# Performance work log

Hardware: AMD Instinct MI355X
Metric: run time of the kernel (lower is better)

## Reference

```python
import jax, jax.numpy as jnp
import numpy as np

N = 6000          # RPN proposals pre-NMS
C = 64            # ROI feature channels
NUM_CLASSES = 21  # VOC-style classes
THR = 0.7         # NMS IoU threshold (generate_rois default)


def setup_inputs() -> dict:
    key = jax.random.key(0)
    k = jax.random.split(key, 8)
    # valid boxes: x1<x2, y1<y2 inside a 1000x1000 image
    xy = jax.random.uniform(k[0], (N, 2)) * 900.0
    wh = jax.random.uniform(k[1], (N, 2)) * 90.0 + 10.0
    boxes = jnp.concatenate([xy, xy + wh], axis=-1)
    scores = jax.random.uniform(k[2], (N,))
    roi_features = jax.random.normal(k[3], (N, 14, 14, C))
    W1 = jax.random.normal(k[4], (2 * 2 * C, 1024)) * 0.02
    b1 = jnp.zeros((1024,))
    Wc = jax.random.normal(k[5], (1024, NUM_CLASSES)) * 0.02
    bc = jnp.zeros((NUM_CLASSES,))
    Wr = jax.random.normal(k[6], (1024, 4)) * 0.02
    br = jnp.zeros((4,))
    return dict(boxes=boxes, scores=scores, roi_features=roi_features,
                W1=W1, b1=b1, Wc=Wc, bc=bc, Wr=Wr, br=br)


def _nms_keep(boxes, scores, thr):
    # Greedy sequential NMS, identical math to the Python loop:
    # highest score kept, suppress any remaining box with IoU >= thr.
    order = jnp.argsort(-scores)
    b = boxes[order]
    x1, y1, x2, y2 = b[:, 0], b[:, 1], b[:, 2], b[:, 3]
    area = (x2 - x1) * (y2 - y1)
    ix1 = jnp.maximum(x1[:, None], x1[None, :])
    iy1 = jnp.maximum(y1[:, None], y1[None, :])
    ix2 = jnp.minimum(x2[:, None], x2[None, :])
    iy2 = jnp.minimum(y2[:, None], y2[None, :])
    inter = jnp.maximum(0.0, ix2 - ix1) * jnp.maximum(0.0, iy2 - iy1)  # [N,N]
    iou = inter / (area[:, None] + area[None, :] - inter)
    n = b.shape[0]
    idx = jnp.arange(n)

    def body(i, keep):
        # if box i survived, suppress later boxes with IoU >= thr
        sup = (iou[i] >= thr) & (idx > i) & keep[i]
        return keep & ~sup

    keep_sorted = jax.lax.fori_loop(0, n, body, jnp.ones(n, dtype=bool))
    return jnp.zeros(n, dtype=bool).at[order].set(keep_sorted)


def reference(boxes, scores, roi_features, W1, b1, Wc, bc, Wr, br):
    keep = _nms_keep(boxes, scores, THR)  # [N] bool, NMS-selected ROIs
    n = roi_features.shape[0]
    # MaxPooling2D(pool_size=7, stride=7): 14x14 -> 2x2
    pooled = roi_features.reshape(n, 2, 7, 2, 7, C).max(axis=(2, 4))
    flat = pooled.reshape(n, -1)                      # [N, 256]
    h = jax.nn.relu(flat @ W1 + b1)                   # [N, 1024]
    cls = jax.nn.softmax(h @ Wc + bc, axis=-1)        # [N, num_classes]
    reg = h @ Wr + br                                 # [N, 4]
    kf = keep.astype(cls.dtype)[:, None]
    # suppressed ROIs zeroed (static-shape stand-in for the variable-length selection)
    return cls * kf, reg * kf, keep
```

## Files before the change

### kernel.cpp

```cpp
#include <hip/hip_runtime.h>

using u64 = unsigned long long;
using u32 = unsigned int;
using u16 = unsigned short;

typedef short bf16x8 __attribute__((ext_vector_type(8)));
typedef float f32x4  __attribute__((ext_vector_type(4)));

#define NB   6000
#define CB94 94
#define THRF 0.7f

__device__ __forceinline__ u16 f2bf(float f) {
    u32 u = __float_as_uint(f);
    return (u16)((u + 0x7FFFu + ((u >> 16) & 1u)) >> 16);
}

__device__ __forceinline__ void gload_lds16(const void* g, void* l) {
    __builtin_amdgcn_global_load_lds((const __attribute__((address_space(1))) void*)g,
                                     (__attribute__((address_space(3))) void*)l, 16, 0, 0);
}


__global__ __launch_bounds__(256) void front_kernel(
        const float* __restrict__ W1, const float* __restrict__ Wc, const float* __restrict__ Wr,
        const float* __restrict__ scores, const float* __restrict__ boxes,
        u16* __restrict__ w1t, u16* __restrict__ w2t,
        int* __restrict__ order, float4* __restrict__ sboxes, u64* __restrict__ bitmap) {
    __shared__ float sj[1024];
    __shared__ int part[4][64];
    int bid = blockIdx.x;
    int t = threadIdx.x;

    if (bid < 1024) {
        int idx = bid * 256 + t;
        int n = idx >> 8, k = idx & 255;
        w1t[idx] = f2bf(W1[k * 1024 + n]);
    } else if (bid < 1152) {
        int idx2 = (bid - 1024) * 256 + t;
        int o = idx2 >> 10, k = idx2 & 1023;
        float v = 0.f;
        if (o < 21) v = Wc[k * 21 + o];
        else if (o < 25) v = Wr[k * 4 + (o - 21)];
        w2t[idx2] = f2bf(v);
    } else {
        int rb = bid - 1152;
        int li = t & 63;
        int q = t >> 6;
        int gi = rb * 64 + li;
        float si = (gi < NB) ? scores[gi] : -1.f;
        int cnt = 0;
        for (int c0 = 0; c0 < NB; c0 += 1024) {
#pragma unroll
            for (int u = 0; u < 4; ++u) {
                int jj = c0 + u * 256 + t;
                sj[u * 256 + t] = (jj < NB) ? scores[jj] : -1e30f;
            }
            __syncthreads();
            int lim = min(1024, NB - c0);
            for (int k = q; k < lim; k += 4) {
                float s = sj[k];
                int j = c0 + k;
                cnt += (s > si) || (s == si && j < gi);
            }
            __syncthreads();
        }
        part[q][li] = cnt;
        __syncthreads();
        if (t < 64 && gi < NB) {
            int r = part[0][t] + part[1][t] + part[2][t] + part[3][t];
            order[r] = gi;
            sboxes[r] = ((const float4*)boxes)[gi];
            bitmap[2 * r] = 0ull;
            bitmap[2 * r + 1] = 0ull;
        }
    }
}


__global__ __launch_bounds__(256) void mask_kernel(const float4* __restrict__ sboxes,
                                                   u64* __restrict__ mask,
                                                   u64* __restrict__ diag,
                                                   u64* __restrict__ bitmap) {
    int cb = blockIdx.x;
    int r0 = blockIdx.y * 256;
    if (cb * 64 + 63 <= r0) return;
    __shared__ float4 cbox[64];
    __shared__ float  carea[64];
    int t = threadIdx.x;
    if (t < 64) {
        int j = cb * 64 + t;
        if (j < NB) {
            float4 b = sboxes[j];
            cbox[t] = b;
            carea[t] = (b.z - b.x) * (b.w - b.y);
        }
    }
    __syncthreads();
    int i = r0 + t;
    if (i >= NB) return;
    float4 a = sboxes[i];
    float aarea = (a.z - a.x) * (a.w - a.y);
    int jn = min(64, NB - cb * 64);
    u64 bits = 0;
    for (int k = 0; k < jn; ++k) {
        int jg = cb * 64 + k;
        if (jg <= i) continue;
        float4 b = cbox[k];
        float iw = fmaxf(fminf(a.z, b.z) - fmaxf(a.x, b.x), 0.f);
        float ih = fmaxf(fminf(a.w, b.w) - fmaxf(a.y, b.y), 0.f);
        float inter = __fmul_rn(iw, ih);
        float denom = __fsub_rn(__fadd_rn(aarea, carea[k]), inter);
        float iou = __fdiv_rn(inter, denom);
        if (iou >= THRF) bits |= 1ull << k;
    }
    mask[(size_t)i * CB94 + cb] = bits;
    if (cb == (i >> 6)) diag[i] = bits;
    if (bits) atomicOr(&bitmap[i * 2 + (cb >> 6)], 1ull << (cb & 63));
}


__global__ __launch_bounds__(256) void scan_kernel(const u64* __restrict__ gmask,
                                                   const u64* __restrict__ gdiag,
                                                   const u64* __restrict__ gbitmap,
                                                   const int* __restrict__ order,
                                                   float* __restrict__ keepF,
                                                   float* __restrict__ out) {
    __shared__ u64 diagLDS[CB94 * 64];
    __shared__ u64 bmLDS[NB * 2];
    __shared__ u64 removedLDS[CB94];
    int t = threadIdx.x;
    for (int idx = t; idx < CB94 * 64; idx += 256)
        diagLDS[idx] = (idx < NB) ? gdiag[idx] : 0ull;
    for (int idx = t; idx < NB * 2; idx += 256) bmLDS[idx] = gbitmap[idx];
    for (int idx = t; idx < CB94; idx += 256) removedLDS[idx] = 0ull;
    __syncthreads();

    if (t < 64) {
        int l = t;
        for (int w = 0; w < CB94; ++w) {
            u64 rm = removedLDS[w];
            u64 dg = diagLDS[w * 64 + l];
            u64 valid = (w == CB94 - 1) ? ((1ull << 48) - 1ull) : ~0ull;
            u64 nz = __ballot(dg != 0ull);
            u64 cand = nz & ~rm & valid;
            while (cand) {
                int b = __ffsll(cand) - 1;
                u64 db = __shfl(dg, b, 64);
                rm |= db;
                cand &= ~rm;
                cand &= ~(1ull << b);
            }
            if (l == 0) removedLDS[w] = rm;
            u64 kept = valid & ~rm;
            if ((kept >> l) & 1ull) {
                int r = w * 64 + l;
                u64 bm0 = bmLDS[2 * r], bm1 = bmLDS[2 * r + 1];
                if (w < 63) bm0 &= ~((2ull << w) - 1ull); else bm0 = 0ull;
                if (w >= 64) bm1 &= ~((2ull << (w - 64)) - 1ull);
                while (bm0) {
                    int tt = __ffsll(bm0) - 1;
                    bm0 &= bm0 - 1;
                    u64 mw = gmask[(size_t)r * CB94 + tt];
                    atomicOr(&removedLDS[tt], mw);
                }
                while (bm1) {
                    int b2 = __ffsll(bm1) - 1;
                    bm1 &= bm1 - 1;
                    int tt = 64 + b2;
                    u64 mw = gmask[(size_t)r * CB94 + tt];
                    atomicOr(&removedLDS[tt], mw);
                }
            }
        }
    }
    __syncthreads();
    for (int k = t; k < NB; k += 256) {
        int sup = (int)((removedLDS[k >> 6] >> (k & 63)) & 1ull);
        float kf = sup ? 0.f : 1.f;
        int orig = order[k];
        keepF[orig] = kf;
        out[150000 + orig] = kf;
    }
}


__global__ __launch_bounds__(256, 4) void pool_kernel(const float* __restrict__ roi,
                                                      u16* __restrict__ flat) {
    int t = threadIdx.x;
    int n = blockIdx.x * 4 + (t >> 6);
    int lane = t & 63;
    int p = lane >> 4, li = lane & 15;
    int ph = p >> 1, pw = p & 1;
    const float4* base = (const float4*)roi + ((size_t)((n * 14 + ph * 7) * 14) + pw * 7) * 16 + li;
    float mx0 = -3.4e38f, mx1 = -3.4e38f, mx2 = -3.4e38f, mx3 = -3.4e38f;
    for (int i = 0; i < 7; ++i) {
        const float4* row = base + (size_t)i * 14 * 16;
        float4 v0 = row[0 * 16], v1 = row[1 * 16], v2 = row[2 * 16], v3 = row[3 * 16];
        float4 v4 = row[4 * 16], v5 = row[5 * 16], v6 = row[6 * 16];
        mx0 = fmaxf(mx0, fmaxf(fmaxf(fmaxf(v0.x, v1.x), fmaxf(v2.x, v3.x)), fmaxf(fmaxf(v4.x, v5.x), v6.x)));
        mx1 = fmaxf(mx1, fmaxf(fmaxf(fmaxf(v0.y, v1.y), fmaxf(v2.y, v3.y)), fmaxf(fmaxf(v4.y, v5.y), v6.y)));
        mx2 = fmaxf(mx2, fmaxf(fmaxf(fmaxf(v0.z, v1.z), fmaxf(v2.z, v3.z)), fmaxf(fmaxf(v4.z, v5.z), v6.z)));
        mx3 = fmaxf(mx3, fmaxf(fmaxf(fmaxf(v0.w, v1.w), fmaxf(v2.w, v3.w)), fmaxf(fmaxf(v4.w, v5.w), v6.w)));
    }
    int ob = n * 256 + p * 64 + li * 4;
    u64 pack = (u64)f2bf(mx0) | ((u64)f2bf(mx1) << 16) | ((u64)f2bf(mx2) << 32) | ((u64)f2bf(mx3) << 48);
    *(u64*)&flat[ob] = pack;
}


__global__ __launch_bounds__(256) void gemm1_kernel(const u16* __restrict__ flat,
                                                    const u16* __restrict__ w1t,
                                                    const float* __restrict__ b1,
                                                    u16* __restrict__ h) {
    __shared__ __align__(16) u16 Alds[128 * 32];
    __shared__ __align__(16) u16 Blds[128 * 32];
    int t = threadIdx.x;
    int c0 = blockIdx.x * 128;
    int r0 = blockIdx.y * 128;
    int lane = t & 63, wid = t >> 6, wr = wid >> 1, wc = wid & 1;
    int lrow = lane & 15, kblk = lane >> 4;
    f32x4 acc[4][4] = {};
    for (int step = 0; step < 8; ++step) {
        int k0 = step * 32;
#pragma unroll
        for (int it = 0; it < 2; ++it) {
            int chunk = it * 256 + t;
            int row = chunk >> 2, kc = chunk & 3;
            int ar = r0 + row; ar = ar < (NB - 1) ? ar : (NB - 1);
            gload_lds16(flat + ar * 256 + k0 + kc * 8, &Alds[chunk * 8]);
            gload_lds16(w1t + (c0 + row) * 256 + k0 + kc * 8, &Blds[chunk * 8]);
        }
        __syncthreads();
        bf16x8 a[4], b[4];
#pragma unroll
        for (int m = 0; m < 4; ++m) a[m] = *(const bf16x8*)&Alds[(wr * 64 + m * 16 + lrow) * 32 + kblk * 8];
#pragma unroll
        for (int n = 0; n < 4; ++n) b[n] = *(const bf16x8*)&Blds[(wc * 64 + n * 16 + lrow) * 32 + kblk * 8];
#pragma unroll
        for (int m = 0; m < 4; ++m)
#pragma unroll
            for (int n = 0; n < 4; ++n)
                acc[m][n] = __builtin_amdgcn_mfma_f32_16x16x32_bf16(a[m], b[n], acc[m][n], 0, 0, 0);
        __syncthreads();
    }
    int rj = lane >> 4;
#pragma unroll
    for (int n = 0; n < 4; ++n) {
        int col = c0 + wc * 64 + n * 16 + lrow;
        float bias = b1[col];
#pragma unroll
        for (int m = 0; m < 4; ++m) {
            int rbase = r0 + wr * 64 + m * 16 + rj * 4;
#pragma unroll
            for (int j = 0; j < 4; ++j) {
                int r = rbase + j;
                if (r < NB) {
                    float v = acc[m][n][j] + bias;
                    v = v > 0.f ? v : 0.f;
                    h[r * 1024 + col] = f2bf(v);
                }
            }
        }
    }
}


__global__ __launch_bounds__(256) void gemm2epi_kernel(const u16* __restrict__ h,
                                                       const u16* __restrict__ w2t,
                                                       const float* __restrict__ keepF,
                                                       const float* __restrict__ bc,
                                                       const float* __restrict__ br,
                                                       float* __restrict__ out) {
    __shared__ __align__(16) u16 Alds[4 * 64 * 32];
    __shared__ __align__(16) u16 Blds[4 * 32 * 32];
    __shared__ float sc[64][33];
    int t = threadIdx.x, lane = t & 63, w = t >> 6;
    int r0 = blockIdx.x * 64;
    int lrow = lane & 15, kblk = lane >> 4;
    f32x4 acc[2] = {};
    for (int round = 0; round < 8; ++round) {
        int kr0 = round * 128;
#pragma unroll
        for (int it = 0; it < 4; ++it) {
            int chunk = it * 256 + t;
            int kk = chunk >> 8, rem = chunk & 255, row = rem >> 2, kc = rem & 3;
            int ar = r0 + row; ar = ar < (NB - 1) ? ar : (NB - 1);
            gload_lds16(h + ar * 1024 + kr0 + kk * 32 + kc * 8, &Alds[chunk * 8]);
        }
#pragma unroll
        for (int it = 0; it < 2; ++it) {
            int chunk = it * 256 + t;
            int kk = chunk >> 7, rem = chunk & 127, orow = rem >> 2, kc = rem & 3;
            gload_lds16(w2t + orow * 1024 + kr0 + kk * 32 + kc * 8, &Blds[chunk * 8]);
        }
        __syncthreads();
#pragma unroll
        for (int kk = 0; kk < 4; ++kk) {
            bf16x8 a = *(const bf16x8*)&Alds[kk * 2048 + (w * 16 + lrow) * 32 + kblk * 8];
#pragma unroll
            for (int nf = 0; nf < 2; ++nf) {
                bf16x8 b = *(const bf16x8*)&Blds[kk * 1024 + (nf * 16 + lrow) * 32 + kblk * 8];
                acc[nf] = __builtin_amdgcn_mfma_f32_16x16x32_bf16(a, b, acc[nf], 0, 0, 0);
            }
        }
        __syncthreads();
    }
#pragma unroll
    for (int nf = 0; nf < 2; ++nf) {
        int col = nf * 16 + lrow;
#pragma unroll
        for (int j = 0; j < 4; ++j) {
            int lr = w * 16 + (lane >> 4) * 4 + j;
            sc[lr][col] = acc[nf][j];
        }
    }
    __syncthreads();
    if (t < 64) {
        int r = r0 + t;
        if (r < NB) {
            float kf = keepF[r];
            float lg[21];
            float m = -3.4e38f;
#pragma unroll
            for (int o = 0; o < 21; ++o) {
                lg[o] = sc[t][o] + bc[o];
                m = fmaxf(m, lg[o]);
            }
            float s = 0.f;
#pragma unroll
            for (int o = 0; o < 21; ++o) {
                lg[o] = expf(lg[o] - m);
                s += lg[o];
            }
            float inv = kf / s;
#pragma unroll
            for (int o = 0; o < 21; ++o) out[r * 21 + o] = lg[o] * inv;
#pragma unroll
            for (int o = 0; o < 4; ++o) out[126000 + r * 4 + o] = (sc[t][21 + o] + br[o]) * kf;
        }
    }
}


extern "C" void kernel_launch(void* const* d_in, const int* in_sizes, int n_in,
                              void* d_out, int out_size, void* d_ws, size_t ws_size,
                              hipStream_t stream) {
    (void)in_sizes; (void)n_in; (void)out_size; (void)ws_size;
    const float* boxes  = (const float*)d_in[0];
    const float* scores = (const float*)d_in[1];
    const float* roi    = (const float*)d_in[2];
    const float* W1     = (const float*)d_in[3];
    const float* b1     = (const float*)d_in[4];
    const float* Wc     = (const float*)d_in[5];
    const float* bc     = (const float*)d_in[6];
    const float* Wr     = (const float*)d_in[7];
    const float* br     = (const float*)d_in[8];
    float* out = (float*)d_out;

    char* ws = (char*)d_ws;
    const size_t O_ORDER  = 0;
    const size_t O_SBOX   = 24064;
    const size_t O_BITMAP = 120064;
    const size_t O_DIAG   = 216064;
    const size_t O_MASK   = 264192;
    const size_t O_KEEPF  = 4776192;
    const size_t O_FLAT   = 4800256;
    const size_t O_W1T    = 7872256;
    const size_t O_W2T    = 8396544;
    const size_t O_H      = 8462080;

    int*    order  = (int*)(ws + O_ORDER);
    float4* sboxes = (float4*)(ws + O_SBOX);
    u64*    bitmap = (u64*)(ws + O_BITMAP);
    u64*    diag   = (u64*)(ws + O_DIAG);
    u64*    mask   = (u64*)(ws + O_MASK);
    float*  keepF  = (float*)(ws + O_KEEPF);
    u16*    flat   = (u16*)(ws + O_FLAT);
    u16*    w1t    = (u16*)(ws + O_W1T);
    u16*    w2t    = (u16*)(ws + O_W2T);
    u16*    h      = (u16*)(ws + O_H);

    front_kernel<<<1246, 256, 0, stream>>>(W1, Wc, Wr, scores, boxes,
                                           w1t, w2t, order, sboxes, bitmap);
    mask_kernel<<<dim3(CB94, 24), 256, 0, stream>>>(sboxes, mask, diag, bitmap);
    scan_kernel<<<1, 256, 0, stream>>>(mask, diag, bitmap, order, keepF, out);
    pool_kernel<<<1500, 256, 0, stream>>>(roi, flat);
    gemm1_kernel<<<dim3(8, 47), 256, 0, stream>>>(flat, w1t, b1, h);
    gemm2epi_kernel<<<CB94, 256, 0, stream>>>(h, w2t, keepF, bc, br, out);
}
```

Before: 235.7 us.

## Compact off-diagonal NMS mask words into an edge list scanned from LDS

The mask kernel now appends every nonzero off-diagonal suppression word to a compact edge list (row/column metadata plus the 64-bit word) through a global atomic counter. The single-block scan kernel loads this list into LDS and, for each column block, ORs the words whose source row is already kept, instead of chasing bitmap entries and issuing dependent global loads of mask words. The goal is to remove latency-bound global reads from the serial greedy scan. When more than EMAX edges exist it falls back to the old path, and the list adds an atomic per nonzero word plus a per-block linear pass over all edges.

```diff
diff --git a/kernel.cpp b/kernel.cpp
--- a/kernel.cpp
+++ b/kernel.cpp
@@ -10,6 +10,7 @@
 #define NB   6000
 #define CB94 94
 #define THRF 0.7f
+#define EMAX 4096
 
 __device__ __forceinline__ u16 f2bf(float f) {
     u32 u = __float_as_uint(f);
@@ -26,13 +27,15 @@
         const float* __restrict__ W1, const float* __restrict__ Wc, const float* __restrict__ Wr,
         const float* __restrict__ scores, const float* __restrict__ boxes,
         u16* __restrict__ w1t, u16* __restrict__ w2t,
-        int* __restrict__ order, float4* __restrict__ sboxes, u64* __restrict__ bitmap) {
+        int* __restrict__ order, float4* __restrict__ sboxes, u64* __restrict__ bitmap,
+        u32* __restrict__ nzcnt) {
     __shared__ float sj[1024];
     __shared__ int part[4][64];
     int bid = blockIdx.x;
     int t = threadIdx.x;
 
     if (bid < 1024) {
+        if (bid == 0 && t == 0) *nzcnt = 0u;
         int idx = bid * 256 + t;
         int n = idx >> 8, k = idx & 255;
         w1t[idx] = f2bf(W1[k * 1024 + n]);
@@ -81,7 +84,10 @@
 __global__ __launch_bounds__(256) void mask_kernel(const float4* __restrict__ sboxes,
                                                    u64* __restrict__ mask,
                                                    u64* __restrict__ diag,
-                                                   u64* __restrict__ bitmap) {
+                                                   u64* __restrict__ bitmap,
+                                                   u32* __restrict__ nzcnt,
+                                                   u32* __restrict__ eMeta,
+                                                   u64* __restrict__ eWord) {
     int cb = blockIdx.x;
     int r0 = blockIdx.y * 256;
     if (cb * 64 + 63 <= r0) return;
@@ -115,31 +121,62 @@
         if (iou >= THRF) bits |= 1ull << k;
     }
     mask[(size_t)i * CB94 + cb] = bits;
-    if (cb == (i >> 6)) diag[i] = bits;
-    if (bits) atomicOr(&bitmap[i * 2 + (cb >> 6)], 1ull << (cb & 63));
-}
-
-
-__global__ __launch_bounds__(256) void scan_kernel(const u64* __restrict__ gmask,
-                                                   const u64* __restrict__ gdiag,
+    if (cb == (i >> 6)) {
+        diag[i] = bits;
+    } else if (bits) {
+        u32 slot = atomicAdd(nzcnt, 1u);
+        if (slot < EMAX) {
+            eMeta[slot] = ((u32)i << 7) | (u32)cb;
+            eWord[slot] = bits;
+        }
+        atomicOr(&bitmap[i * 2 + (cb >> 6)], 1ull << (cb & 63));
+    }
+}
+
+
+__global__ __launch_bounds__(256) void scan_kernel(const u64* __restrict__ gdiag,
+                                                   const u32* __restrict__ gMeta,
+                                                   const u64* __restrict__ gWord,
+                                                   const u32* __restrict__ nzcnt,
+                                                   const u64* __restrict__ gmask,
                                                    const u64* __restrict__ gbitmap,
                                                    const int* __restrict__ order,
                                                    float* __restrict__ keepF,
                                                    float* __restrict__ out) {
     __shared__ u64 diagLDS[CB94 * 64];
-    __shared__ u64 bmLDS[NB * 2];
+    __shared__ u64 eW[EMAX];
+    __shared__ u32 eM[EMAX];
+    __shared__ u64 keptLDS[CB94];
     __shared__ u64 removedLDS[CB94];
     int t = threadIdx.x;
+    int Eg = (int)*nzcnt;
+    bool fb = (Eg > EMAX);
+    int E = fb ? 0 : Eg;
     for (int idx = t; idx < CB94 * 64; idx += 256)
         diagLDS[idx] = (idx < NB) ? gdiag[idx] : 0ull;
-    for (int idx = t; idx < NB * 2; idx += 256) bmLDS[idx] = gbitmap[idx];
-    for (int idx = t; idx < CB94; idx += 256) removedLDS[idx] = 0ull;
+    for (int idx = t; idx < E; idx += 256) { eM[idx] = gMeta[idx]; eW[idx] = gWord[idx]; }
+    for (int idx = t; idx < CB94; idx += 256) { removedLDS[idx] = 0ull; keptLDS[idx] = 0ull; }
     __syncthreads();
 
     if (t < 64) {
         int l = t;
         for (int w = 0; w < CB94; ++w) {
-            u64 rm = removedLDS[w];
+            u64 rm;
+            if (!fb) {
+                u64 myOr = 0ull;
+                for (int e = l; e < E; e += 64) {
+                    u32 m = eM[e];
+                    if ((m & 127u) == (u32)w) {
+                        int r = (int)(m >> 7);
+                        if ((keptLDS[r >> 6] >> (r & 63)) & 1ull) myOr |= eW[e];
+                    }
+                }
+#pragma unroll
+                for (int off = 32; off; off >>= 1) myOr |= __shfl_xor(myOr, off, 64);
+                rm = myOr;
+            } else {
+                rm = removedLDS[w];
+            }
             u64 dg = diagLDS[w * 64 + l];
             u64 valid = (w == CB94 - 1) ? ((1ull << 48) - 1ull) : ~0ull;
             u64 nz = __ballot(dg != 0ull);
@@ -151,11 +188,14 @@
                 cand &= ~rm;
                 cand &= ~(1ull << b);
             }
-            if (l == 0) removedLDS[w] = rm;
             u64 kept = valid & ~rm;
-            if ((kept >> l) & 1ull) {
+            if (l == 0) {
+                removedLDS[w] = rm;
+                keptLDS[w] = kept;
+            }
+            if (fb && ((kept >> l) & 1ull)) {
                 int r = w * 64 + l;
-                u64 bm0 = bmLDS[2 * r], bm1 = bmLDS[2 * r + 1];
+                u64 bm0 = gbitmap[2 * r], bm1 = gbitmap[2 * r + 1];
                 if (w < 63) bm0 &= ~((2ull << w) - 1ull); else bm0 = 0ull;
                 if (w >= 64) bm1 &= ~((2ull << (w - 64)) - 1ull);
                 while (bm0) {
@@ -365,10 +405,13 @@
     const size_t O_DIAG   = 216064;
     const size_t O_MASK   = 264192;
     const size_t O_KEEPF  = 4776192;
-    const size_t O_FLAT   = 4800256;
-    const size_t O_W1T    = 7872256;
-    const size_t O_W2T    = 8396544;
-    const size_t O_H      = 8462080;
+    const size_t O_NZCNT  = 4800256;
+    const size_t O_EMETA  = 4800320;
+    const size_t O_EWORD  = 4816704;
+    const size_t O_FLAT   = 4849472;
+    const size_t O_W1T    = 7921472;
+    const size_t O_W2T    = 8445760;
+    const size_t O_H      = 8511296;
 
     int*    order  = (int*)(ws + O_ORDER);
     float4* sboxes = (float4*)(ws + O_SBOX);
@@ -376,15 +419,18 @@
     u64*    diag   = (u64*)(ws + O_DIAG);
     u64*    mask   = (u64*)(ws + O_MASK);
     float*  keepF  = (float*)(ws + O_KEEPF);
+    u32*    nzcnt  = (u32*)(ws + O_NZCNT);
+    u32*    eMeta  = (u32*)(ws + O_EMETA);
+    u64*    eWord  = (u64*)(ws + O_EWORD);
     u16*    flat   = (u16*)(ws + O_FLAT);
     u16*    w1t    = (u16*)(ws + O_W1T);
     u16*    w2t    = (u16*)(ws + O_W2T);
     u16*    h      = (u16*)(ws + O_H);
 
     front_kernel<<<1246, 256, 0, stream>>>(W1, Wc, Wr, scores, boxes,
-                                           w1t, w2t, order, sboxes, bitmap);
-    mask_kernel<<<dim3(CB94, 24), 256, 0, stream>>>(sboxes, mask, diag, bitmap);
-    scan_kernel<<<1, 256, 0, stream>>>(mask, diag, bitmap, order, keepF, out);
+                                           w1t, w2t, order, sboxes, bitmap, nzcnt);
+    mask_kernel<<<dim3(CB94, 24), 256, 0, stream>>>(sboxes, mask, diag, bitmap, nzcnt, eMeta, eWord);
+    scan_kernel<<<1, 256, 0, stream>>>(diag, eMeta, eWord, nzcnt, mask, bitmap, order, keepF, out);
     pool_kernel<<<1500, 256, 0, stream>>>(roi, flat);
     gemm1_kernel<<<dim3(8, 47), 256, 0, stream>>>(flat, w1t, b1, h);
     gemm2epi_kernel<<<CB94, 256, 0, stream>>>(h, w2t, keepF, bc, br, out);
```

Measured after the change: 257.5 us. 9.2% more time.
